# Kernel tuning notes

Hardware: AMD Instinct MI355X
Metric: run time of the kernel (lower is better)

The kernel has to match this reference:

```python
import jax, jax.numpy as jnp
import numpy as np

MASK_DENSITY = 0.1  # fraction of nonzero weights kept by the sparsity mask


def setup_inputs() -> dict:
    key = jax.random.key(0)
    k_data, k_w, k_m, k_b = jax.random.split(key, 4)
    tokens, in_f, out_f = 8192, 4096, 4096
    data = jax.random.normal(k_data, (tokens, in_f), dtype=jnp.float32)
    weight = jax.random.normal(k_w, (out_f, in_f), dtype=jnp.float32)
    mask = (jax.random.uniform(k_m, (out_f, in_f)) < MASK_DENSITY).astype(jnp.float32)
    bias = jax.random.normal(k_b, (out_f,), dtype=jnp.float32)
    return {"data": data, "weight": weight, "mask": mask, "bias": bias}


def reference(data, weight, mask, bias):
    # out = data @ (mask * weight)^T + bias  (sparse linear; CSR of mask*weight
    # in the original kernel -- dense math is identical).
    w_sp = mask * weight                      # [out_f, in_f]
    out = jnp.einsum("ti,oi->to", data, w_sp) # [tokens, out_f]
    return out + bias
```

## Files before the change

kernel.cpp:

```cpp
#include <hip/hip_runtime.h>
#include <hip/hip_bf16.h>


#define GM 8192
#define GN 4096
#define GK 4096
#define NT (GK / 32)

typedef __attribute__((ext_vector_type(8))) short short8;
typedef __attribute__((ext_vector_type(8))) short bf16x8;
typedef __attribute__((ext_vector_type(4))) float f32x4;

__device__ __forceinline__ short f2bf(float x) {
    unsigned u = __builtin_bit_cast(unsigned, x);
    u += 0x7fffu + ((u >> 16) & 1u);
    return (short)(u >> 16);
}

__device__ __forceinline__ void stage16(const short* g, short* l) {
    __builtin_amdgcn_global_load_lds(
        (const __attribute__((address_space(1))) unsigned int*)g,
        (__attribute__((address_space(3))) unsigned int*)l, 16, 0, 0);
}

__global__ void cvt_data_kernel(const float* __restrict__ in, short* __restrict__ out, long n) {
    long i0 = ((long)blockIdx.x * blockDim.x + threadIdx.x) * 8;
    long stride = (long)gridDim.x * blockDim.x * 8;
    for (long i = i0; i < n; i += stride) {
        float4 a = *(const float4*)(in + i);
        float4 b = *(const float4*)(in + i + 4);
        short8 o;
        o[0] = f2bf(a.x); o[1] = f2bf(a.y); o[2] = f2bf(a.z); o[3] = f2bf(a.w);
        o[4] = f2bf(b.x); o[5] = f2bf(b.y); o[6] = f2bf(b.z); o[7] = f2bf(b.w);
        *(short8*)(out + i) = o;
    }
}

__global__ void cvt_w_kernel(const float* __restrict__ w, const float* __restrict__ m,
                             short* __restrict__ out, long n) {
    long i0 = ((long)blockIdx.x * blockDim.x + threadIdx.x) * 8;
    long stride = (long)gridDim.x * blockDim.x * 8;
    for (long i = i0; i < n; i += stride) {
        float4 wa = *(const float4*)(w + i);
        float4 wb = *(const float4*)(w + i + 4);
        float4 ma = *(const float4*)(m + i);
        float4 mb = *(const float4*)(m + i + 4);
        short8 o;
        o[0] = f2bf(wa.x * ma.x); o[1] = f2bf(wa.y * ma.y);
        o[2] = f2bf(wa.z * ma.z); o[3] = f2bf(wa.w * ma.w);
        o[4] = f2bf(wb.x * mb.x); o[5] = f2bf(wb.y * mb.y);
        o[6] = f2bf(wb.z * mb.z); o[7] = f2bf(wb.w * mb.w);
        *(short8*)(out + i) = o;
    }
}

__global__ __launch_bounds__(512, 2) void gemm_8w(const short* __restrict__ A,
                                                  const short* __restrict__ B,
                                                  const float* __restrict__ bias,
                                                  float* __restrict__ C) {
    __shared__ short lds[65536];

    const int tid  = threadIdx.x;
    const int lane = tid & 63;
    const int wid  = tid >> 6;
    const int wr   = wid >> 2;
    const int wc   = wid & 3;

    const int bid  = blockIdx.x;
    const int swz  = (bid & 7) * 64 + (bid >> 3);
    const int brow = (swz >> 4) << 8;
    const int bcol = (swz & 15) << 8;

    const int lrow  = tid >> 2;
    const int q_log = (tid & 3) ^ ((((lrow >> 3) & 1) << 1) | ((lrow >> 1) & 1));
    const size_t aSrc0 = (size_t)(brow + lrow) * GK + q_log * 8;
    const size_t bSrc0 = (size_t)(bcol + lrow) * GK + q_log * 8;

    const int l15 = lane & 15;
    const int q   = lane >> 4;
    const int qx  = (((l15 >> 3) & 1) << 1) | ((l15 >> 1) & 1);
    const int foff = l15 * 32 + ((q ^ qx) << 3);
    const int aOff = wr * 4096 + foff;
    const int bOff = 8192 + (wc >> 1) * 4096 + (wc & 1) * 2048 + foff;

    f32x4 acc[8][4] = {};

    auto stageA = [&](int t) {
        const int ring = (t & 3) * 16384;
        const size_t k = (size_t)t * 32;
        #pragma unroll
        for (int h = 0; h < 2; ++h)
            stage16(A + aSrc0 + (size_t)h * 128 * GK + k, &lds[ring + h * 4096 + wid * 512]);
    };
    auto stageB = [&](int t) {
        const int ring = (t & 3) * 16384;
        const size_t k = (size_t)t * 32;
        #pragma unroll
        for (int h = 0; h < 2; ++h)
            stage16(B + bSrc0 + (size_t)h * 128 * GK + k, &lds[ring + 8192 + h * 4096 + wid * 512]);
    };

    stageA(0); stageB(0);
    stageA(1); stageB(1);
    stageA(2); stageB(2);
    asm volatile("s_waitcnt vmcnt(8)" ::: "memory");
    __builtin_amdgcn_s_barrier();

    for (int T = 0; T < NT; ++T) {
        const int ring = (T & 3) * 16384;
        bf16x8 af[4], bf[4];

        #pragma unroll
        for (int m = 0; m < 4; ++m) af[m] = *(const bf16x8*)&lds[ring + aOff + m * 512];
        #pragma unroll
        for (int n = 0; n < 4; ++n) bf[n] = *(const bf16x8*)&lds[ring + bOff + n * 512];
        if (T + 3 < NT) stageA(T + 3);
        __builtin_amdgcn_s_barrier();
        asm volatile("s_waitcnt lgkmcnt(0)" ::: "memory");
        __builtin_amdgcn_sched_barrier(0);
        __builtin_amdgcn_s_setprio(1);
        #pragma unroll
        for (int m = 0; m < 4; ++m)
            #pragma unroll
            for (int n = 0; n < 4; ++n)
                acc[m][n] = __builtin_amdgcn_mfma_f32_16x16x32_bf16(af[m], bf[n], acc[m][n], 0, 0, 0);
        __builtin_amdgcn_s_setprio(0);
        __builtin_amdgcn_s_barrier();

        #pragma unroll
        for (int m = 0; m < 4; ++m) af[m] = *(const bf16x8*)&lds[ring + aOff + (m + 4) * 512];
        if (T + 3 < NT) stageB(T + 3);
        __builtin_amdgcn_s_barrier();
        asm volatile("s_waitcnt lgkmcnt(0)" ::: "memory");
        __builtin_amdgcn_sched_barrier(0);
        __builtin_amdgcn_s_setprio(1);
        #pragma unroll
        for (int m = 0; m < 4; ++m)
            #pragma unroll
            for (int n = 0; n < 4; ++n)
                acc[m + 4][n] = __builtin_amdgcn_mfma_f32_16x16x32_bf16(af[m], bf[n], acc[m + 4][n], 0, 0, 0);
        __builtin_amdgcn_s_setprio(0);

        if (T < NT - 3)       { asm volatile("s_waitcnt vmcnt(8)" ::: "memory"); }
        else if (T == NT - 3) { asm volatile("s_waitcnt vmcnt(4)" ::: "memory"); }
        else if (T == NT - 2) { asm volatile("s_waitcnt vmcnt(0)" ::: "memory"); }
        __builtin_amdgcn_s_barrier();
    }

    #pragma unroll
    for (int n = 0; n < 4; ++n) {
        const int col = bcol + wc * 64 + n * 16 + l15;
        const float bv = bias[col];
        #pragma unroll
        for (int m = 0; m < 8; ++m) {
            const int rowb = brow + wr * 128 + m * 16 + (q << 2);
            #pragma unroll
            for (int r = 0; r < 4; ++r)
                C[(size_t)(rowb + r) * GN + col] = acc[m][n][r] + bv;
        }
    }
}

extern "C" void kernel_launch(void* const* d_in, const int* in_sizes, int n_in,
                              void* d_out, int out_size, void* d_ws, size_t ws_size,
                              hipStream_t stream) {
    const float* data   = (const float*)d_in[0];
    const float* weight = (const float*)d_in[1];
    const float* mask   = (const float*)d_in[2];
    const float* bias   = (const float*)d_in[3];
    float* out = (float*)d_out;

    short* dataB = (short*)d_ws;
    short* wB    = dataB + (size_t)GM * GK;

    cvt_data_kernel<<<2048, 256, 0, stream>>>(data, dataB, (long)GM * GK);
    cvt_w_kernel<<<2048, 256, 0, stream>>>(weight, mask, wB, (long)GN * GK);

    gemm_8w<<<512, 512, 0, stream>>>(dataB, wB, bias, out);
}
```

Baseline: 310.0 us.

## Double-buffer MFMA fragments in registers and cut barriers to one per tile

The K loop is unrolled by two with ping-pong register fragments. The next tile's LDS fragment reads are issued before the second half of the current tile's MFMAs, so they overlap compute. The three per-tile workgroup barriers become one, and the global-load wait moves from vmcnt(8) to vmcnt(4) so the next ring slot is guaranteed resident. This adds register pressure for the extra fragment buffers and leaves less slack on outstanding global loads.

```diff
diff --git a/kernel.cpp b/kernel.cpp
--- a/kernel.cpp
+++ b/kernel.cpp
@@ -84,6 +84,7 @@
     const int bOff = 8192 + (wc >> 1) * 4096 + (wc & 1) * 2048 + foff;
 
     f32x4 acc[8][4] = {};
+    bf16x8 afA[4], afB[4], bfA[4], bfB[4];
 
     auto stageA = [&](int t) {
         const int ring = (t & 3) * 16384;
@@ -103,49 +104,60 @@
     stageA(0); stageB(0);
     stageA(1); stageB(1);
     stageA(2); stageB(2);
-    asm volatile("s_waitcnt vmcnt(8)" ::: "memory");
+    asm volatile("s_waitcnt vmcnt(4)" ::: "memory");
     __builtin_amdgcn_s_barrier();
+    asm volatile("" ::: "memory");
+    #pragma unroll
+    for (int m = 0; m < 4; ++m) afA[m] = *(const bf16x8*)&lds[aOff + m * 512];
+    #pragma unroll
+    for (int n = 0; n < 4; ++n) bfA[n] = *(const bf16x8*)&lds[bOff + n * 512];
 
-    for (int T = 0; T < NT; ++T) {
-        const int ring = (T & 3) * 16384;
-        bf16x8 af[4], bf[4];
+#define TILE_BODY(T, AF_P0, AF_P1, BF_CUR, BF_NXT)                                 \
+  {                                                                                 \
+    const int ring  = ((T) & 3) * 16384;                                            \
+    const int ringN = (((T) + 1) & 3) * 16384;                                      \
+                                                             \
+    if ((T) + 3 < NT) stageA((T) + 3);                                              \
+    _Pragma("unroll")                                                               \
+    for (int m = 0; m < 4; ++m)                                                     \
+      AF_P1[m] = *(const bf16x8*)&lds[ring + aOff + (m + 4) * 512];                 \
+    __builtin_amdgcn_sched_barrier(0);                                              \
+    __builtin_amdgcn_s_setprio(1);                                                  \
+    _Pragma("unroll")                                                               \
+    for (int m = 0; m < 4; ++m)                                                     \
+      _Pragma("unroll")                                                             \
+      for (int n = 0; n < 4; ++n)                                                   \
+        acc[m][n] = __builtin_amdgcn_mfma_f32_16x16x32_bf16(AF_P0[m], BF_CUR[n],    \
+                                                            acc[m][n], 0, 0, 0);    \
+    __builtin_amdgcn_s_setprio(0);                                                  \
+       \
+    if ((T) + 3 < NT) stageB((T) + 3);                                              \
+    _Pragma("unroll")                                                               \
+    for (int m = 0; m < 4; ++m)                                                     \
+      AF_P0[m] = *(const bf16x8*)&lds[ringN + aOff + m * 512];                      \
+    _Pragma("unroll")                                                               \
+    for (int n = 0; n < 4; ++n)                                                     \
+      BF_NXT[n] = *(const bf16x8*)&lds[ringN + bOff + n * 512];                     \
+    __builtin_amdgcn_sched_barrier(0);                                              \
+    __builtin_amdgcn_s_setprio(1);                                                  \
+    _Pragma("unroll")                                                               \
+    for (int m = 0; m < 4; ++m)                                                     \
+      _Pragma("unroll")                                                             \
+      for (int n = 0; n < 4; ++n)                                                   \
+        acc[m + 4][n] = __builtin_amdgcn_mfma_f32_16x16x32_bf16(AF_P1[m], BF_CUR[n],\
+                                                                acc[m + 4][n], 0, 0, 0); \
+    __builtin_amdgcn_s_setprio(0);                                                  \
+    if ((T) + 3 < NT) { asm volatile("s_waitcnt vmcnt(4)" ::: "memory"); }          \
+    else              { asm volatile("s_waitcnt vmcnt(0)" ::: "memory"); }          \
+    __builtin_amdgcn_s_barrier();                                                   \
+    asm volatile("" ::: "memory");                                                  \
+  }
 
-        #pragma unroll
-        for (int m = 0; m < 4; ++m) af[m] = *(const bf16x8*)&lds[ring + aOff + m * 512];
-        #pragma unroll
-        for (int n = 0; n < 4; ++n) bf[n] = *(const bf16x8*)&lds[ring + bOff + n * 512];
-        if (T + 3 < NT) stageA(T + 3);
-        __builtin_amdgcn_s_barrier();
-        asm volatile("s_waitcnt lgkmcnt(0)" ::: "memory");
-        __builtin_amdgcn_sched_barrier(0);
-        __builtin_amdgcn_s_setprio(1);
-        #pragma unroll
-        for (int m = 0; m < 4; ++m)
-            #pragma unroll
-            for (int n = 0; n < 4; ++n)
-                acc[m][n] = __builtin_amdgcn_mfma_f32_16x16x32_bf16(af[m], bf[n], acc[m][n], 0, 0, 0);
-        __builtin_amdgcn_s_setprio(0);
-        __builtin_amdgcn_s_barrier();
-
-        #pragma unroll
-        for (int m = 0; m < 4; ++m) af[m] = *(const bf16x8*)&lds[ring + aOff + (m + 4) * 512];
-        if (T + 3 < NT) stageB(T + 3);
-        __builtin_amdgcn_s_barrier();
-        asm volatile("s_waitcnt lgkmcnt(0)" ::: "memory");
-        __builtin_amdgcn_sched_barrier(0);
-        __builtin_amdgcn_s_setprio(1);
-        #pragma unroll
-        for (int m = 0; m < 4; ++m)
-            #pragma unroll
-            for (int n = 0; n < 4; ++n)
-                acc[m + 4][n] = __builtin_amdgcn_mfma_f32_16x16x32_bf16(af[m], bf[n], acc[m + 4][n], 0, 0, 0);
-        __builtin_amdgcn_s_setprio(0);
-
-        if (T < NT - 3)       { asm volatile("s_waitcnt vmcnt(8)" ::: "memory"); }
-        else if (T == NT - 3) { asm volatile("s_waitcnt vmcnt(4)" ::: "memory"); }
-        else if (T == NT - 2) { asm volatile("s_waitcnt vmcnt(0)" ::: "memory"); }
-        __builtin_amdgcn_s_barrier();
+    for (int T = 0; T < NT; T += 2) {
+        TILE_BODY(T,     afA, afB, bfA, bfB);
+        TILE_BODY(T + 1, afA, afB, bfB, bfA);
     }
+#undef TILE_BODY
 
     #pragma unroll
     for (int n = 0; n < 4; ++n) {
```

Result: faster. 296.7 us (-4.3%).

## Switch GEMM LDS pipeline from 4-stage K=32 ring to double-buffered K=64

Applied to the files above, without the earlier changes.

Replaces the four-slot ring of 32-wide K tiles, three in flight, with two 32K-short buffers each holding a 64-wide K tile split into two 32-wide sub-blocks. Each main-loop iteration now runs four compute phases and prefetches the next 64-wide tile into the other buffer one sub-block at a time. This halves the outer-loop trip count and spreads the global-to-LDS staging more evenly across phases. In exchange, prefetch depth drops from three tiles ahead to one, which could expose more global-memory latency.

```diff
diff --git a/kernel.cpp b/kernel.cpp
--- a/kernel.cpp
+++ b/kernel.cpp
@@ -5,7 +5,7 @@
 #define GM 8192
 #define GN 4096
 #define GK 4096
-#define NT (GK / 32)
+#define NT (GK / 64)
 
 typedef __attribute__((ext_vector_type(8))) short short8;
 typedef __attribute__((ext_vector_type(8))) short bf16x8;
@@ -71,81 +71,82 @@
     const int brow = (swz >> 4) << 8;
     const int bcol = (swz & 15) << 8;
 
-    const int lrow  = tid >> 2;
-    const int q_log = (tid & 3) ^ ((((lrow >> 3) & 1) << 1) | ((lrow >> 1) & 1));
-    const size_t aSrc0 = (size_t)(brow + lrow) * GK + q_log * 8;
-    const size_t bSrc0 = (size_t)(bcol + lrow) * GK + q_log * 8;
+    const int trow = tid >> 2;
+    const int qlog = (tid & 3) ^ ((((trow >> 3) & 1) << 1) | ((trow >> 1) & 1));
 
     const int l15 = lane & 15;
     const int q   = lane >> 4;
     const int qx  = (((l15 >> 3) & 1) << 1) | ((l15 >> 1) & 1);
     const int foff = l15 * 32 + ((q ^ qx) << 3);
-    const int aOff = wr * 4096 + foff;
-    const int bOff = 8192 + (wc >> 1) * 4096 + (wc & 1) * 2048 + foff;
+    const int aW = wr * 4096;
+    const int bW = wc * 2048;
 
     f32x4 acc[8][4] = {};
+    bf16x8 af[4], bfr[4];
 
-    auto stageA = [&](int t) {
-        const int ring = (t & 3) * 16384;
-        const size_t k = (size_t)t * 32;
+    auto stA = [&](int kb, int sb, size_t kcol) {
         #pragma unroll
-        for (int h = 0; h < 2; ++h)
-            stage16(A + aSrc0 + (size_t)h * 128 * GK + k, &lds[ring + h * 4096 + wid * 512]);
+        for (int j = 0; j < 2; ++j)
+            stage16(A + (size_t)(brow + j * 128 + trow) * GK + kcol + kb * 32 + qlog * 8,
+                    &lds[sb + kb * 8192 + j * 4096 + wid * 512]);
     };
-    auto stageB = [&](int t) {
-        const int ring = (t & 3) * 16384;
-        const size_t k = (size_t)t * 32;
+    auto stB = [&](int kb, int sb, size_t kcol) {
         #pragma unroll
-        for (int h = 0; h < 2; ++h)
-            stage16(B + bSrc0 + (size_t)h * 128 * GK + k, &lds[ring + 8192 + h * 4096 + wid * 512]);
+        for (int j = 0; j < 2; ++j)
+            stage16(B + (size_t)(bcol + j * 128 + trow) * GK + kcol + kb * 32 + qlog * 8,
+                    &lds[sb + 16384 + kb * 8192 + j * 4096 + wid * 512]);
     };
 
-    stageA(0); stageB(0);
-    stageA(1); stageB(1);
-    stageA(2); stageB(2);
-    asm volatile("s_waitcnt vmcnt(8)" ::: "memory");
+    stA(0, 0, 0); stB(0, 0, 0); stA(1, 0, 0); stB(1, 0, 0);
+    asm volatile("s_waitcnt vmcnt(4)" ::: "memory");
     __builtin_amdgcn_s_barrier();
+    asm volatile("" ::: "memory");
+
+#define PHASE(KB, MH, VMSTMT, STGSTMT)                                            \
+  {                                                                                \
+    VMSTMT;                                                                        \
+    _Pragma("unroll")                                                              \
+    for (int m = 0; m < 4; ++m)                                                    \
+      af[m] = *(const bf16x8*)&lds[cb + (KB) * 8192 + aW + ((MH) * 4 + m) * 512 + foff]; \
+    if ((MH) == 0) {                                                               \
+      _Pragma("unroll")                                                            \
+      for (int n = 0; n < 4; ++n)                                                  \
+        bfr[n] = *(const bf16x8*)&lds[cb + 16384 + (KB) * 8192 + bW + n * 512 + foff]; \
+    }                                                                              \
+    STGSTMT;                                                                       \
+    __builtin_amdgcn_s_barrier();                                                  \
+    asm volatile("s_waitcnt lgkmcnt(0)" ::: "memory");                             \
+    __builtin_amdgcn_sched_barrier(0);                                             \
+    __builtin_amdgcn_s_setprio(1);                                                 \
+    _Pragma("unroll")                                                              \
+    for (int m = 0; m < 4; ++m)                                                    \
+      _Pragma("unroll")                                                            \
+      for (int n = 0; n < 4; ++n)                                                  \
+        acc[(MH) * 4 + m][n] = __builtin_amdgcn_mfma_f32_16x16x32_bf16(            \
+            af[m], bfr[n], acc[(MH) * 4 + m][n], 0, 0, 0);                         \
+    __builtin_amdgcn_s_setprio(0);                                                 \
+    __builtin_amdgcn_s_barrier();                                                  \
+    asm volatile("" ::: "memory");                                                 \
+  }
 
     for (int T = 0; T < NT; ++T) {
-        const int ring = (T & 3) * 16384;
-        bf16x8 af[4], bf[4];
+        const int cb = (T & 1) << 15;
+        const int sb = 32768 - cb;
+        const size_t kn = (size_t)(T + 1) * 64;
+        const bool st = (T + 1 < NT);
 
-        #pragma unroll
-        for (int m = 0; m < 4; ++m) af[m] = *(const bf16x8*)&lds[ring + aOff + m * 512];
-        #pragma unroll
-        for (int n = 0; n < 4; ++n) bf[n] = *(const bf16x8*)&lds[ring + bOff + n * 512];
-        if (T + 3 < NT) stageA(T + 3);
-        __builtin_amdgcn_s_barrier();
-        asm volatile("s_waitcnt lgkmcnt(0)" ::: "memory");
-        __builtin_amdgcn_sched_barrier(0);
-        __builtin_amdgcn_s_setprio(1);
-        #pragma unroll
-        for (int m = 0; m < 4; ++m)
-            #pragma unroll
-            for (int n = 0; n < 4; ++n)
-                acc[m][n] = __builtin_amdgcn_mfma_f32_16x16x32_bf16(af[m], bf[n], acc[m][n], 0, 0, 0);
-        __builtin_amdgcn_s_setprio(0);
-        __builtin_amdgcn_s_barrier();
-
-        #pragma unroll
-        for (int m = 0; m < 4; ++m) af[m] = *(const bf16x8*)&lds[ring + aOff + (m + 4) * 512];
-        if (T + 3 < NT) stageB(T + 3);
-        __builtin_amdgcn_s_barrier();
-        asm volatile("s_waitcnt lgkmcnt(0)" ::: "memory");
-        __builtin_amdgcn_sched_barrier(0);
-        __builtin_amdgcn_s_setprio(1);
-        #pragma unroll
-        for (int m = 0; m < 4; ++m)
-            #pragma unroll
-            for (int n = 0; n < 4; ++n)
-                acc[m + 4][n] = __builtin_amdgcn_mfma_f32_16x16x32_bf16(af[m], bf[n], acc[m + 4][n], 0, 0, 0);
-        __builtin_amdgcn_s_setprio(0);
-
-        if (T < NT - 3)       { asm volatile("s_waitcnt vmcnt(8)" ::: "memory"); }
-        else if (T == NT - 3) { asm volatile("s_waitcnt vmcnt(4)" ::: "memory"); }
-        else if (T == NT - 2) { asm volatile("s_waitcnt vmcnt(0)" ::: "memory"); }
-        __builtin_amdgcn_s_barrier();
+        PHASE(0, 0, , if (st) stA(0, sb, kn))
+        PHASE(0, 1,
+              if (st) { asm volatile("s_waitcnt vmcnt(2)" ::: "memory"); }
+              else    { asm volatile("s_waitcnt vmcnt(0)" ::: "memory"); },
+              if (st) stB(0, sb, kn))
+        PHASE(1, 0, , if (st) stA(1, sb, kn))
+        PHASE(1, 1,
+              if (st) { asm volatile("s_waitcnt vmcnt(2)" ::: "memory"); }
+              else    { asm volatile("s_waitcnt vmcnt(0)" ::: "memory"); },
+              if (st) stB(1, sb, kn))
     }
+#undef PHASE
 
     #pragma unroll
     for (int n = 0; n < 4; ++n) {
```

Result: faster. 298.2 us (-3.8%).
